# Optimization experiments

Hardware: AMD Instinct MI355X
Metric: run time of the kernel (lower is better)

Reference implementation:

```python
import jax, jax.numpy as jnp
import numpy as np
from jax import lax

C = 173            # EEG channels (independent towers)
L = 400            # samples per channel
POOL_OUT = 10      # AdaptiveMaxPool1d output length (400/10 = 40 exact window)
EPS = 1e-5


def setup_inputs() -> dict:
    key = jax.random.key(0)
    ks = jax.random.split(key, 6)
    B = 64
    x = jax.random.normal(ks[0], (B, C, L), dtype=jnp.float32)
    # per-channel tower 1: Conv1d(1,16,9)  -> grouped kernel [C*16, 1, 9]
    w1 = jax.random.normal(ks[1], (C * 16, 1, 9), dtype=jnp.float32) * 0.2
    b1 = jnp.zeros((C * 16,), jnp.float32)
    g1 = jnp.ones((C * 16,), jnp.float32)
    beta1 = jnp.zeros((C * 16,), jnp.float32)
    m1 = jnp.zeros((C * 16,), jnp.float32)
    v1 = jnp.ones((C * 16,), jnp.float32)
    # per-channel tower 2: Conv1d(16,32,7) -> grouped kernel [C*32, 16, 7]
    w2 = jax.random.normal(ks[2], (C * 32, 16, 7), dtype=jnp.float32) * 0.05
    b2 = jnp.zeros((C * 32,), jnp.float32)
    g2 = jnp.ones((C * 32,), jnp.float32)
    beta2 = jnp.zeros((C * 32,), jnp.float32)
    m2 = jnp.zeros((C * 32,), jnp.float32)
    v2 = jnp.ones((C * 32,), jnp.float32)
    # combiner MLP: Linear(32*C*10, 128) -> ReLU -> Linear(128, 1)
    wc1 = jax.random.normal(ks[3], (128, 32 * C * POOL_OUT), dtype=jnp.float32) * 0.01
    bc1 = jnp.zeros((128,), jnp.float32)
    wc2 = jax.random.normal(ks[4], (1, 128), dtype=jnp.float32) * 0.05
    bc2 = jnp.zeros((1,), jnp.float32)
    return dict(x=x, w1=w1, b1=b1, g1=g1, beta1=beta1, m1=m1, v1=v1,
                w2=w2, b2=b2, g2=g2, beta2=beta2, m2=m2, v2=v2,
                wc1=wc1, bc1=bc1, wc2=wc2, bc2=bc2)


def _bn(y, g, beta, m, v):
    # inference-mode BatchNorm1d over channel axis of [B, CF, L]
    inv = g * lax.rsqrt(v + EPS)
    return y * inv[None, :, None] + (beta - m * inv)[None, :, None]


def reference(x, w1, b1, g1, beta1, m1, v1, w2, b2, g2, beta2, m2, v2, wc1, bc1, wc2, bc2):
    B = x.shape[0]
    dn = ('NCH', 'OIH', 'NCH')
    # tower conv 1: all 173 per-channel Conv1d(1,16,9,pad=4) as one grouped conv
    y = lax.conv_general_dilated(x, w1, (1,), [(4, 4)], dimension_numbers=dn,
                                 feature_group_count=C)           # [B, C*16, 400]
    y = jax.nn.relu(_bn(y + b1[None, :, None], g1, beta1, m1, v1))
    # tower conv 2: Conv1d(16,32,7,pad=3), grouped by channel
    y = lax.conv_general_dilated(y, w2, (1,), [(3, 3)], dimension_numbers=dn,
                                 feature_group_count=C)           # [B, C*32, 400]
    y = jax.nn.relu(_bn(y + b2[None, :, None], g2, beta2, m2, v2))
    # AdaptiveMaxPool1d(10): exact non-overlapping windows of 40
    y = y.reshape(B, C * 32, POOL_OUT, L // POOL_OUT).max(axis=-1)  # [B, C*32, 10]
    # concat of per-channel flattened features == flatten (channel, feat, pos)
    flat = y.reshape(B, C * 32 * POOL_OUT)                          # [B, 55360]
    h = jax.nn.relu(flat @ wc1.T + bc1)
    out = h @ wc2.T + bc2                                           # [B, 1]
    return out
```

## Files before the change

### kernel.cpp

```cpp
#include <hip/hip_runtime.h>

#define C_CH 173
#define L_IN 400
#define EPSV 1e-5f
#define KFEAT 55360

typedef __fp16   fp16x2 __attribute__((ext_vector_type(2)));
typedef _Float16 f16x8  __attribute__((ext_vector_type(8)));
typedef float    f32x4  __attribute__((ext_vector_type(4)));
typedef float    f32x16 __attribute__((ext_vector_type(16)));

#define Y1T_STRIDE_I 9
#define Y1T_ROWS   406

#define SEG_STRIDE 102

#define N1 (173 * 3584)
#define N2 (173 * 512)
#define N3 (173 * 96)

__global__ __launch_bounds__(256) void prep_kernel(
    const float* __restrict__ w1, const float* __restrict__ b1,
    const float* __restrict__ g1, const float* __restrict__ beta1,
    const float* __restrict__ m1, const float* __restrict__ v1,
    const float* __restrict__ w2, const float* __restrict__ b2,
    const float* __restrict__ g2, const float* __restrict__ beta2,
    const float* __restrict__ m2, const float* __restrict__ v2,
    _Float16* __restrict__ w2T_g, _Float16* __restrict__ w1T_g,
    float* __restrict__ sc_g)
{
    const int idx = blockIdx.x * 256 + threadIdx.x;
    if (idx < N1) {
        int c = idx / 3584, r = idx - c * 3584;
        int dt = r >> 9, fg = r & 511;
        int f = fg >> 4, g = fg & 15;
        w2T_g[idx] = (_Float16)w2[c * 3584 + f * 112 + g * 7 + dt];
    } else if (idx < N1 + N2) {
        int j = idx - N1;
        int c = j / 512, r = j - c * 512;
        int g = r >> 5, k = r & 31;
        w1T_g[j] = (k < 9) ? (_Float16)w1[c * 144 + g * 9 + k] : (_Float16)0.0f;
    } else if (idx < N1 + N2 + N3) {
        int j = idx - N1 - N2;
        int c = j / 96, r = j - c * 96;
        float o;
        if (r < 32) {
            int g  = r & 15;
            int cf = c * 16 + g;
            float inv = g1[cf] * rsqrtf(v1[cf] + EPSV);
            o = (r < 16) ? inv : (b1[cf] - m1[cf]) * inv + beta1[cf];
        } else {
            int f  = (r - 32) & 31;
            int cf = c * 32 + f;
            float inv = g2[cf] * rsqrtf(v2[cf] + EPSV);
            o = (r < 64) ? inv : (b2[cf] - m2[cf]) * inv + beta2[cf];
        }
        sc_g[j] = o;
    }
}

__global__ __launch_bounds__(320, 8) void tower_kernel(
    const float* __restrict__ x,
    const _Float16* __restrict__ w2T_g, const _Float16* __restrict__ w1T_g,
    const float* __restrict__ sc_g,
    _Float16* __restrict__ featH)
{
    __shared__ __align__(16) _Float16 xa_s[432];
    __shared__ __align__(16) _Float16 xb_s[432];
    __shared__ __align__(16) _Float16 w1T_s[16 * 32];
    __shared__ __align__(16) _Float16 y1T_s[Y1T_ROWS * 2 * Y1T_STRIDE_I];
    __shared__ __align__(16) _Float16 w2T_s[7 * 512];
    __shared__ _Float16               segmax_s[32 * SEG_STRIDE];
    __shared__ __align__(16) float    cst_s[96];

    const int c   = blockIdx.x;
    const int tid = threadIdx.x;

    {
        const int4* w2src = (const int4*)(w2T_g + (size_t)c * 3584);
        for (int i = tid; i < 448; i += 320) ((int4*)w2T_s)[i] = w2src[i];
        const int4* w1src = (const int4*)(w1T_g + c * 512);
        if (tid < 64) ((int4*)w1T_s)[tid] = w1src[tid];
        const float4* csrc = (const float4*)(sc_g + c * 96);
        if (tid >= 64 && tid < 88) ((float4*)cst_s)[tid - 64] = csrc[tid - 64];
        if (tid >= 88 && tid < 142) {
            int i = tid - 88;
            int r = i / 9, cx = i - r * 9;
            int row = (r < 3) ? r : (400 + r);
            ((int*)y1T_s)[row * Y1T_STRIDE_I + cx] = 0;
        }
    }
    __syncthreads();
    const float s2f  = cst_s[32 + (tid & 31)];
    const float sh2f = cst_s[64 + (tid & 31)];

    for (int nb = 0; nb < 4; ++nb) {
        const int b = blockIdx.y * 4 + nb;

        const float* xrow = x + ((size_t)b * C_CH + c) * L_IN;
        for (int i = tid; i < 432; i += 320) {
            float v = (i >= 4 && i < 404) ? xrow[i - 4] : 0.0f;
            _Float16 h = (_Float16)v;
            xa_s[i] = h;
            if (i > 0) xb_s[i - 1] = h;
        }
        if (tid == 0) xb_s[431] = (_Float16)0.0f;
        __syncthreads();

        {
            const int lane = tid & 63;
            const int wv5  = tid >> 6;
            const int nl   = lane & 15;
            const int q    = lane >> 4;
            union { int4 v; f16x8 h; } a1;
            a1.v = *(const int4*)((const int*)w1T_s + nl * 16 + q * 4);
            float s1r[4], sh1r[4];
#pragma unroll
            for (int r = 0; r < 4; ++r) {
                s1r[r]  = cst_s[q * 4 + r];
                sh1r[r] = cst_s[16 + q * 4 + r];
            }
            const int* xsel = (const int*)((nl & 1) ? xb_s : xa_s);
            for (int tile = 0; tile < 5; ++tile) {
                const int t0 = (wv5 * 5 + tile) * 16;
                const int dw = (t0 + nl + q * 8) >> 1;
                union { int4 v; f16x8 h; } bf;
                bf.v.x = xsel[dw];
                bf.v.y = xsel[dw + 1];
                bf.v.z = xsel[dw + 2];
                bf.v.w = xsel[dw + 3];
                f32x4 acc = {0.0f, 0.0f, 0.0f, 0.0f};
                acc = __builtin_amdgcn_mfma_f32_16x16x32_f16(a1.h, bf.h, acc, 0, 0, 0);
                union { _Float16 h[4]; int2 d; } pk;
#pragma unroll
                for (int r = 0; r < 4; ++r) {
                    float v = acc[r] * s1r[r] + sh1r[r];
                    pk.h[r] = (_Float16)(v > 0.0f ? v : 0.0f);
                }
                int* yp = (int*)y1T_s + (t0 + nl + 3) * Y1T_STRIDE_I + q * 2;
                yp[0] = pk.d.x;
                yp[1] = pk.d.y;
            }
        }
        __syncthreads();

        {
            const int wv    = tid >> 6;
            const int lane  = tid & 63;
            const int nlane = lane & 31;
            const int half  = lane >> 5;

            union F8q { int4 q; f16x8 h; } af[7];
#pragma unroll
            for (int dt = 0; dt < 7; ++dt)
                af[dt].q = *(const int4*)((const int*)w2T_s + dt * 256 + nlane * 8 + half * 4);

            for (int tile = wv; tile < 13; tile += 5) {
                const int tA  = tile * 32 + nlane;
                const int tAr = tA < 400 ? tA : 399;
                f32x16 acc;
#pragma unroll
                for (int i = 0; i < 16; ++i) acc[i] = 0.0f;

#pragma unroll
                for (int dt = 0; dt < 7; ++dt) {
                    const int* p = (const int*)y1T_s + (tAr + dt) * Y1T_STRIDE_I + half * 4;
                    union { int d[4]; f16x8 h; } bf;
                    bf.d[0] = p[0];
                    bf.d[1] = p[1];
                    bf.d[2] = p[2];
                    bf.d[3] = p[3];
                    acc = __builtin_amdgcn_mfma_f32_32x32x16_f16(bf.h, af[dt].h, acc, 0, 0, 0);
                }

                const int base = nlane * SEG_STRIDE + tile * 8 + half;
#pragma unroll
                for (int q = 0; q < 4; ++q) {
                    float v0 = acc[4 * q + 0] * s2f;
                    float v1 = acc[4 * q + 1] * s2f;
                    float v2 = acc[4 * q + 2] * s2f;
                    float v3 = acc[4 * q + 3] * s2f;
                    float m  = fmaxf(fmaxf(v0, v1), fmaxf(v2, v3));
                    const int sub = tile * 8 + 2 * q + half;
                    if (sub < 100) segmax_s[base + 2 * q] = (_Float16)m;
                }
            }
        }
        __syncthreads();

        {
            const int f = tid & 31;
            const int p = tid >> 5;
            float m = -3.0e38f;
#pragma unroll
            for (int k = 0; k < 10; ++k)
                m = fmaxf(m, (float)segmax_s[f * SEG_STRIDE + p * 10 + k]);
            float v = fmaxf(m + sh2f, 0.0f);
            featH[(size_t)b * KFEAT + (c * 32 + f) * 10 + p] = (_Float16)v;
        }
    }
}

__global__ __launch_bounds__(256) void fc1_kernel(
    const _Float16* __restrict__ featH, const float* __restrict__ wc1,
    float* __restrict__ part)
{
    const int tid   = threadIdx.x;
    const int kb    = blockIdx.x;
    const int k0    = kb * 320;
    const int lane  = tid & 63;
    const int wv    = tid >> 6;
    const int nlane = lane & 31;
    const int half  = lane >> 5;
    const int jrow  = wv * 32 + nlane;

    const float*    ap  = wc1   + (size_t)jrow * KFEAT + k0 + half * 8;
    const _Float16* b0p = featH + (size_t)nlane * KFEAT + k0 + half * 8;
    const _Float16* b1p = featH + (size_t)(nlane + 32) * KFEAT + k0 + half * 8;

    f32x16 acc0, acc1;
#pragma unroll
    for (int i = 0; i < 16; ++i) { acc0[i] = 0.0f; acc1[i] = 0.0f; }

#pragma unroll 2
    for (int s = 0; s < 20; ++s) {
        const float4 aw0 = *(const float4*)(ap + s * 16);
        const float4 aw1 = *(const float4*)(ap + s * 16 + 4);
        union { fp16x2 v2[4]; f16x8 h; } a;
        a.v2[0] = __builtin_amdgcn_cvt_pkrtz(aw0.x, aw0.y);
        a.v2[1] = __builtin_amdgcn_cvt_pkrtz(aw0.z, aw0.w);
        a.v2[2] = __builtin_amdgcn_cvt_pkrtz(aw1.x, aw1.y);
        a.v2[3] = __builtin_amdgcn_cvt_pkrtz(aw1.z, aw1.w);

        union { int4 q; f16x8 h; } b0, b1;
        b0.q = *(const int4*)(b0p + s * 16);
        b1.q = *(const int4*)(b1p + s * 16);

        acc0 = __builtin_amdgcn_mfma_f32_32x32x16_f16(a.h, b0.h, acc0, 0, 0, 0);
        acc1 = __builtin_amdgcn_mfma_f32_32x32x16_f16(a.h, b1.h, acc1, 0, 0, 0);
    }

    float* pt = part + (size_t)kb * 8192;
#pragma unroll
    for (int reg = 0; reg < 16; ++reg) {
        int j = wv * 32 + (reg & 3) + 8 * (reg >> 2) + 4 * half;
        pt[j * 64 + nlane]      = acc0[reg];
        pt[j * 64 + 32 + nlane] = acc1[reg];
    }
}

__global__ __launch_bounds__(256) void reduce_kernel(
    const float* __restrict__ part, float* __restrict__ h_ws)
{
    const int idx = blockIdx.x * 256 + threadIdx.x;
    float s = 0.0f;
    for (int kb = 0; kb < 173; ++kb)
        s += part[(size_t)kb * 8192 + idx];
    h_ws[idx] = s;
}

__global__ __launch_bounds__(64) void fc2_kernel(
    const float* __restrict__ h_ws, const float* __restrict__ bc1,
    const float* __restrict__ wc2, const float* __restrict__ bc2,
    float* __restrict__ out)
{
    const int b = threadIdx.x;
    float acc = bc2[0];
    for (int j = 0; j < 128; ++j) {
        float hv = h_ws[j * 64 + b] + bc1[j];
        hv = hv > 0.0f ? hv : 0.0f;
        acc += wc2[j] * hv;
    }
    out[b] = acc;
}

extern "C" void kernel_launch(void* const* d_in, const int* in_sizes, int n_in,
                              void* d_out, int out_size, void* d_ws, size_t ws_size,
                              hipStream_t stream)
{
    const float* x     = (const float*)d_in[0];
    const float* w1    = (const float*)d_in[1];
    const float* b1    = (const float*)d_in[2];
    const float* g1    = (const float*)d_in[3];
    const float* beta1 = (const float*)d_in[4];
    const float* m1    = (const float*)d_in[5];
    const float* v1    = (const float*)d_in[6];
    const float* w2    = (const float*)d_in[7];
    const float* b2    = (const float*)d_in[8];
    const float* g2    = (const float*)d_in[9];
    const float* beta2 = (const float*)d_in[10];
    const float* m2    = (const float*)d_in[11];
    const float* v2    = (const float*)d_in[12];
    const float* wc1   = (const float*)d_in[13];
    const float* bc1   = (const float*)d_in[14];
    const float* wc2   = (const float*)d_in[15];
    const float* bc2   = (const float*)d_in[16];

    char* ws = (char*)d_ws;
    _Float16* featH = (_Float16*)ws;
    float*    part  = (float*)(ws + 7086080);
    float*    h_ws  = (float*)(ws + 12754944);
    _Float16* w2T_g = (_Float16*)(ws + 12787712);
    _Float16* w1T_g = (_Float16*)(ws + 14027776);
    float*    sc_g  = (float*)(ws + 14204928);

    hipLaunchKernelGGL(prep_kernel, dim3(2834), dim3(256), 0, stream,
                       w1, b1, g1, beta1, m1, v1,
                       w2, b2, g2, beta2, m2, v2, w2T_g, w1T_g, sc_g);

    hipLaunchKernelGGL(tower_kernel, dim3(C_CH, 16), dim3(320), 0, stream,
                       x, w2T_g, w1T_g, sc_g, featH);

    hipLaunchKernelGGL(fc1_kernel, dim3(173), dim3(256), 0, stream,
                       featH, wc1, part);

    hipLaunchKernelGGL(reduce_kernel, dim3(32), dim3(256), 0, stream,
                       part, h_ws);

    hipLaunchKernelGGL(fc2_kernel, dim3(1), dim3(64), 0, stream,
                       h_ws, bc1, wc2, bc2, (float*)d_out);
}
```

Measured before the change: 209.3 us.

## Fuse reduce and fc2 kernels, hoist w2 fragments, tweak occupancy and unroll

Merges the split-K reduction and the final 128->1 layer into one kernel with one block per batch element, which drops a launch and the h_ws round trip. The tower kernel now loads its w2 MFMA fragments into registers once per block rather than once per batch iteration, and its launch-bounds occupancy hint goes from 8 to 7 to give more register room. The fc1 inner loop unroll rises from 2 to 4. The fused reduction reads the partial sums with a 64-float stride per thread, so its loads may coalesce worse than the old reduce kernel's.

```diff
diff --git a/kernel.cpp b/kernel.cpp
--- a/kernel.cpp
+++ b/kernel.cpp
@@ -59,7 +59,7 @@
     }
 }
 
-__global__ __launch_bounds__(320, 8) void tower_kernel(
+__global__ __launch_bounds__(320, 7) void tower_kernel(
     const float* __restrict__ x,
     const _Float16* __restrict__ w2T_g, const _Float16* __restrict__ w1T_g,
     const float* __restrict__ sc_g,
@@ -93,6 +93,13 @@
     __syncthreads();
     const float s2f  = cst_s[32 + (tid & 31)];
     const float sh2f = cst_s[64 + (tid & 31)];
+
+    const int nlaneH = tid & 31;
+    const int halfH  = (tid >> 5) & 1;
+    union F8q { int4 q; f16x8 h; } af[7];
+#pragma unroll
+    for (int dt = 0; dt < 7; ++dt)
+        af[dt].q = *(const int4*)((const int*)w2T_s + dt * 256 + nlaneH * 8 + halfH * 4);
 
     for (int nb = 0; nb < 4; ++nb) {
         const int b = blockIdx.y * 4 + nb;
@@ -146,14 +153,8 @@
 
         {
             const int wv    = tid >> 6;
-            const int lane  = tid & 63;
-            const int nlane = lane & 31;
-            const int half  = lane >> 5;
-
-            union F8q { int4 q; f16x8 h; } af[7];
-#pragma unroll
-            for (int dt = 0; dt < 7; ++dt)
-                af[dt].q = *(const int4*)((const int*)w2T_s + dt * 256 + nlane * 8 + half * 4);
+            const int nlane = nlaneH;
+            const int half  = halfH;
 
             for (int tile = wv; tile < 13; tile += 5) {
                 const int tA  = tile * 32 + nlane;
@@ -222,7 +223,7 @@
 #pragma unroll
     for (int i = 0; i < 16; ++i) { acc0[i] = 0.0f; acc1[i] = 0.0f; }
 
-#pragma unroll 2
+#pragma unroll 4
     for (int s = 0; s < 20; ++s) {
         const float4 aw0 = *(const float4*)(ap + s * 16);
         const float4 aw1 = *(const float4*)(ap + s * 16 + 4);
@@ -249,29 +250,48 @@
     }
 }
 
-__global__ __launch_bounds__(256) void reduce_kernel(
-    const float* __restrict__ part, float* __restrict__ h_ws)
-{
-    const int idx = blockIdx.x * 256 + threadIdx.x;
-    float s = 0.0f;
-    for (int kb = 0; kb < 173; ++kb)
-        s += part[(size_t)kb * 8192 + idx];
-    h_ws[idx] = s;
-}
-
-__global__ __launch_bounds__(64) void fc2_kernel(
-    const float* __restrict__ h_ws, const float* __restrict__ bc1,
+__global__ __launch_bounds__(256) void reduce_fc2_kernel(
+    const float* __restrict__ part, const float* __restrict__ bc1,
     const float* __restrict__ wc2, const float* __restrict__ bc2,
     float* __restrict__ out)
 {
-    const int b = threadIdx.x;
-    float acc = bc2[0];
-    for (int j = 0; j < 128; ++j) {
-        float hv = h_ws[j * 64 + b] + bc1[j];
-        hv = hv > 0.0f ? hv : 0.0f;
-        acc += wc2[j] * hv;
-    }
-    out[b] = acc;
+    __shared__ float hsum[256];
+    __shared__ float vsum[128];
+
+    const int b = blockIdx.x;
+    const int t = threadIdx.x;
+    const int j = t >> 1;
+    const int kh = t & 1;
+
+    const float* p = part + (size_t)j * 64 + b;
+    const int kb0 = kh ? 87 : 0;
+    const int kb1 = kh ? 173 : 87;
+    float s = 0.0f;
+#pragma unroll 4
+    for (int kb = kb0; kb < kb1; ++kb)
+        s += p[(size_t)kb * 8192];
+    hsum[t] = s;
+    __syncthreads();
+
+    float v = 0.0f;
+    if (t < 128) {
+        float h = hsum[t * 2] + hsum[t * 2 + 1] + bc1[t];
+        h = h > 0.0f ? h : 0.0f;
+        v = wc2[t] * h;
+        vsum[t] = v;
+    }
+    __syncthreads();
+
+    if (t < 64) {
+        float r = vsum[t] + vsum[t + 64];
+        r += __shfl_down(r, 32);
+        r += __shfl_down(r, 16);
+        r += __shfl_down(r, 8);
+        r += __shfl_down(r, 4);
+        r += __shfl_down(r, 2);
+        r += __shfl_down(r, 1);
+        if (t == 0) out[b] = r + bc2[0];
+    }
 }
 
 extern "C" void kernel_launch(void* const* d_in, const int* in_sizes, int n_in,
@@ -299,7 +319,6 @@
     char* ws = (char*)d_ws;
     _Float16* featH = (_Float16*)ws;
     float*    part  = (float*)(ws + 7086080);
-    float*    h_ws  = (float*)(ws + 12754944);
     _Float16* w2T_g = (_Float16*)(ws + 12787712);
     _Float16* w1T_g = (_Float16*)(ws + 14027776);
     float*    sc_g  = (float*)(ws + 14204928);
@@ -314,9 +333,6 @@
     hipLaunchKernelGGL(fc1_kernel, dim3(173), dim3(256), 0, stream,
                        featH, wc1, part);
 
-    hipLaunchKernelGGL(reduce_kernel, dim3(32), dim3(256), 0, stream,
-                       part, h_ws);
-
-    hipLaunchKernelGGL(fc2_kernel, dim3(1), dim3(64), 0, stream,
-                       h_ws, bc1, wc2, bc2, (float*)d_out);
-}
+    hipLaunchKernelGGL(reduce_fc2_kernel, dim3(64), dim3(256), 0, stream,
+                       part, bc1, wc2, bc2, (float*)d_out);
+}
```

Result: no change. 209.1 us (-0.1%).
